# Kernel tuning notes

Hardware: AMD Instinct MI355X
Metric: run time of the kernel (lower is better)

The kernel has to match this reference:

```python
import jax, jax.numpy as jnp
import numpy as np


def _avgpool2(x):
    # 2x2 average pool, stride 2, NHWC
    B, H, W, C = x.shape
    return x.reshape(B, H // 2, 2, W // 2, 2, C).mean(axis=(2, 4))


def setup_inputs() -> dict:
    key = jax.random.key(0)
    ks = jax.random.split(key, 5)
    B, H, W, C = 8, 64, 64, 512
    s = 0.02
    return {
        "x": jax.random.normal(ks[0], (B, H, W, C), dtype=jnp.float32),
        "wf": jax.random.normal(ks[1], (C, C // 8), dtype=jnp.float32) * s,
        "wg": jax.random.normal(ks[2], (C, C // 8), dtype=jnp.float32) * s,
        "wh": jax.random.normal(ks[3], (C, C // 2), dtype=jnp.float32) * s,
        "wo": jax.random.normal(ks[4], (C // 2, C), dtype=jnp.float32) * s,
    }


def reference(x, wf, wg, wh, wo):
    B, H, W, C = x.shape
    # queries from full resolution: 1x1 conv == channel matmul
    f = jnp.einsum("bhwc,cd->bhwd", x, wf).reshape(B, H * W, C // 8)
    # keys/values from 2x2 average-pooled map
    xp = _avgpool2(x)  # [B, H/2, W/2, C]
    g = jnp.einsum("bhwc,cd->bhwd", xp, wg).reshape(B, H * W // 4, C // 8)
    h = jnp.einsum("bhwc,cd->bhwd", xp, wh).reshape(B, H * W // 4, C // 2)
    # attn: [B, HW, HW/4], softmax over pooled key axis
    attn = jax.nn.softmax(jnp.einsum("bnd,bmd->bnm", f, g), axis=-1)
    y = jnp.einsum("bnm,bmd->bnd", attn, h).reshape(B, H, W, C // 2)
    # output 1x1 conv back to C channels
    return jnp.einsum("bhwc,cd->bhwd", y, wo)
```

## Files before the change

### kernel.cpp

```cpp
#include <hip/hip_runtime.h>
#include <hip/hip_bf16.h>

typedef __attribute__((ext_vector_type(8))) short bshort8;
typedef __attribute__((ext_vector_type(4))) float f32x4;
typedef __attribute__((ext_vector_type(4))) float vfloat4;
typedef __attribute__((ext_vector_type(4))) unsigned int vuint4;
typedef __attribute__((ext_vector_type(2))) unsigned int vuint2;

__device__ __forceinline__ unsigned short f2bf(float f) {
    union { float f; unsigned u; } v; v.f = f;
    unsigned u = v.u;
    u += 0x7fffu + ((u >> 16) & 1u);
    return (unsigned short)(u >> 16);
}

template<int EPI>
__global__ __launch_bounds__(256)
void gemm_bt(const unsigned short* __restrict__ Av, const unsigned short* __restrict__ Btv,
             void* __restrict__ Cv,
             int M, int N, int K,
             long long aB, long long bB, long long cB)
{
    __shared__ __align__(128) char sA[64 * 64];
    __shared__ __align__(128) char sB[64 * 64];

    const int b    = blockIdx.z;
    const int tid  = threadIdx.x;
    const int bRow = blockIdx.y << 6;
    const int bCol = blockIdx.x << 6;
    const int wid  = tid >> 6, lane = tid & 63;
    const int wr   = wid >> 1, wc   = wid & 1;
    const int r16  = lane & 15, kg  = lane >> 4;
    const int srow = tid >> 2,  skc = tid & 3;

    const unsigned short* A  = Av  + (size_t)aB * b;
    const unsigned short* Bt = Btv + (size_t)bB * b;

    f32x4 acc[2][2] = {};

    const size_t aRowBase = (size_t)(bRow + srow) * K + skc * 8;
    const size_t bRowBase = (size_t)(bCol + srow) * K + skc * 8;
    const unsigned swW = ((((unsigned)srow) << 6) | (((unsigned)skc) << 4))
                         ^ ((((unsigned)srow) & 7u) << 4);

    for (int k0 = 0; k0 < K; k0 += 32) {
        vuint4 apack = *(const vuint4*)(A  + aRowBase + k0);
        vuint4 bpack = *(const vuint4*)(Bt + bRowBase + k0);
        *(vuint4*)(sA + swW) = apack;
        *(vuint4*)(sB + swW) = bpack;
        __syncthreads();

        bshort8 af[2], bfr[2];
        #pragma unroll
        for (int mi = 0; mi < 2; mi++) {
            unsigned row = (unsigned)(wr * 32 + mi * 16 + r16);
            unsigned off = ((row << 6) | (((unsigned)kg) << 4)) ^ ((row & 7u) << 4);
            af[mi] = *(const bshort8*)(sA + off);
        }
        #pragma unroll
        for (int ni = 0; ni < 2; ni++) {
            unsigned col = (unsigned)(wc * 32 + ni * 16 + r16);
            unsigned off = ((col << 6) | (((unsigned)kg) << 4)) ^ ((col & 7u) << 4);
            bfr[ni] = *(const bshort8*)(sB + off);
        }
        #pragma unroll
        for (int mi = 0; mi < 2; mi++)
            #pragma unroll
            for (int ni = 0; ni < 2; ni++)
                acc[mi][ni] = __builtin_amdgcn_mfma_f32_16x16x32_bf16(
                                  af[mi], bfr[ni], acc[mi][ni], 0, 0, 0);
        __syncthreads();
    }

    #pragma unroll
    for (int mi = 0; mi < 2; mi++) {
        const int row0 = bRow + wr * 32 + mi * 16 + kg * 4;
        #pragma unroll
        for (int ni = 0; ni < 2; ni++) {
            const int col = bCol + wc * 32 + ni * 16 + r16;
            #pragma unroll
            for (int r = 0; r < 4; r++) {
                const int row = row0 + r;
                float x = acc[mi][ni][r];
                const size_t ci = (size_t)cB * b + (size_t)row * N + col;
                if constexpr (EPI == 0) ((float*)Cv)[ci] = x;
                else                    ((unsigned short*)Cv)[ci] = f2bf(x);
            }
        }
    }
}

__global__ __launch_bounds__(512)
void flash_attn(const float* __restrict__ x,
                const unsigned short* __restrict__ wft,
                const unsigned short* __restrict__ gb,
                const unsigned short* __restrict__ ht,
                unsigned short* __restrict__ yb)
{
    __shared__ __align__(128) char sS[128 * 128];
    __shared__ __align__(128) char sG[64 * 128];
    __shared__ __align__(128) char sH[256 * 128];
    __shared__ float rs[128];

    const int tid = threadIdx.x;
    const int bid = blockIdx.x;
    const int b   = bid & 7;
    const int q0  = (bid >> 3) << 7;
    const int wid = tid >> 6, lane = tid & 63;
    const int wr  = wid >> 1, wc = wid & 1;
    const int r16 = lane & 15, kg = lane >> 4;

    const float*          xB = x  + ((size_t)b * 4096 + q0) * 512;
    const unsigned short* gB = gb + (size_t)b * 1024 * 64;
    const unsigned short* hB = ht + (size_t)b * 256 * 1024;

    f32x4 facc[4] = {};
    {
        const int xrow = tid >> 2, xc = tid & 3;
        const int wrow = tid >> 3, wkc = tid & 7;
        const int frow = wid << 4;
        for (int k0 = 0; k0 < 512; k0 += 64) {
            {
                const float* p = xB + (size_t)xrow * 512 + k0 + xc * 16;
                #pragma unroll
                for (int j = 0; j < 2; j++) {
                    vfloat4 a0 = *(const vfloat4*)(p + j * 8);
                    vfloat4 a1 = *(const vfloat4*)(p + j * 8 + 4);
                    vuint4 w;
                    w[0] = (unsigned)f2bf(a0[0]) | ((unsigned)f2bf(a0[1]) << 16);
                    w[1] = (unsigned)f2bf(a0[2]) | ((unsigned)f2bf(a0[3]) << 16);
                    w[2] = (unsigned)f2bf(a1[0]) | ((unsigned)f2bf(a1[1]) << 16);
                    w[3] = (unsigned)f2bf(a1[2]) | ((unsigned)f2bf(a1[3]) << 16);
                    unsigned off = ((unsigned)xrow * 128 + (unsigned)(xc * 32 + j * 16))
                                   ^ (((unsigned)xrow & 7u) << 4);
                    *(vuint4*)(sH + off) = w;
                }
            }
            {
                vuint4 v = *(const vuint4*)(wft + (size_t)wrow * 512 + k0 + wkc * 8);
                unsigned off = ((unsigned)wrow * 128 + (unsigned)wkc * 16)
                               ^ (((unsigned)wrow & 7u) << 4);
                *(vuint4*)(sG + off) = v;
            }
            __syncthreads();

            bshort8 ax[2];
            {
                unsigned row = (unsigned)(frow + r16);
                unsigned base = row * 128, sw = (row & 7u) << 4;
                ax[0] = *(const bshort8*)(sH + ((base + (unsigned)kg * 16) ^ sw));
                ax[1] = *(const bshort8*)(sH + ((base + 64 + (unsigned)kg * 16) ^ sw));
            }
            #pragma unroll
            for (int ni = 0; ni < 4; ni++) {
                unsigned col = (unsigned)(ni * 16 + r16);
                unsigned base = col * 128, sw = (col & 7u) << 4;
                bshort8 b0 = *(const bshort8*)(sG + ((base + (unsigned)kg * 16) ^ sw));
                bshort8 b1 = *(const bshort8*)(sG + ((base + 64 + (unsigned)kg * 16) ^ sw));
                facc[ni] = __builtin_amdgcn_mfma_f32_16x16x32_bf16(ax[0], b0, facc[ni], 0, 0, 0);
                facc[ni] = __builtin_amdgcn_mfma_f32_16x16x32_bf16(ax[1], b1, facc[ni], 0, 0, 0);
            }
            __syncthreads();
        }

        #pragma unroll
        for (int ni = 0; ni < 4; ni++) {
            const unsigned col = (unsigned)(ni * 16 + r16);
            #pragma unroll
            for (int r = 0; r < 4; r++) {
                unsigned row = (unsigned)(frow + kg * 4 + r);
                unsigned off = (row * 128 + col * 2) ^ ((row & 7u) << 4);
                *(unsigned short*)(sS + off) = f2bf(facc[ni][r]);
            }
        }
    }
    __syncthreads();

    bshort8 af[2][2];
    #pragma unroll
    for (int mi = 0; mi < 2; mi++) {
        unsigned row = (unsigned)(wr * 32 + mi * 16 + r16);
        unsigned base = row * 128, sw = (row & 7u) << 4;
        af[mi][0] = *(const bshort8*)(sS + ((base + (unsigned)kg * 16) ^ sw));
        af[mi][1] = *(const bshort8*)(sS + ((base + 64 + (unsigned)kg * 16) ^ sw));
    }

    f32x4 yacc[2][8] = {};
    float psum[2][4] = {};
    const int kc = tid & 7, n0 = tid >> 3;

    for (int c = 0; c < 16; c++) {
        const int kv0 = c << 6;
        {
            vuint4 v = *(const vuint4*)(gB + (size_t)(kv0 + n0) * 64 + kc * 8);
            unsigned off = ((unsigned)n0 * 128 + (unsigned)kc * 16) ^ (((unsigned)n0 & 7u) << 4);
            *(vuint4*)(sG + off) = v;
        }
        #pragma unroll
        for (int it = 0; it < 4; it++) {
            const int n = n0 + it * 64;
            vuint4 v = *(const vuint4*)(hB + (size_t)n * 1024 + kv0 + kc * 8);
            unsigned off = ((unsigned)n * 128 + (unsigned)kc * 16) ^ (((unsigned)n & 7u) << 4);
            *(vuint4*)(sH + off) = v;
        }
        __syncthreads();

        f32x4 sacc[2][2] = {};
        #pragma unroll
        for (int ni = 0; ni < 2; ni++) {
            unsigned col = (unsigned)(wc * 32 + ni * 16 + r16);
            unsigned base = col * 128, sw = (col & 7u) << 4;
            bshort8 g0 = *(const bshort8*)(sG + ((base + (unsigned)kg * 16) ^ sw));
            bshort8 g1 = *(const bshort8*)(sG + ((base + 64 + (unsigned)kg * 16) ^ sw));
            #pragma unroll
            for (int mi = 0; mi < 2; mi++) {
                sacc[mi][ni] = __builtin_amdgcn_mfma_f32_16x16x32_bf16(af[mi][0], g0, sacc[mi][ni], 0, 0, 0);
                sacc[mi][ni] = __builtin_amdgcn_mfma_f32_16x16x32_bf16(af[mi][1], g1, sacc[mi][ni], 0, 0, 0);
            }
        }

        #pragma unroll
        for (int mi = 0; mi < 2; mi++)
            #pragma unroll
            for (int ni = 0; ni < 2; ni++) {
                const unsigned col = (unsigned)(wc * 32 + ni * 16 + r16);
                #pragma unroll
                for (int r = 0; r < 4; r++) {
                    float e = __expf(sacc[mi][ni][r]);
                    psum[mi][r] += e;
                    unsigned row = (unsigned)(wr * 32 + mi * 16 + kg * 4 + r);
                    unsigned off = (row * 128 + col * 2) ^ ((row & 7u) << 4);
                    *(unsigned short*)(sS + off) = f2bf(e);
                }
            }
        __syncthreads();

        bshort8 pa[2][2];
        #pragma unroll
        for (int mi = 0; mi < 2; mi++) {
            unsigned row = (unsigned)(wr * 32 + mi * 16 + r16);
            unsigned base = row * 128, sw = (row & 7u) << 4;
            pa[mi][0] = *(const bshort8*)(sS + ((base + (unsigned)kg * 16) ^ sw));
            pa[mi][1] = *(const bshort8*)(sS + ((base + 64 + (unsigned)kg * 16) ^ sw));
        }
        #pragma unroll
        for (int ni = 0; ni < 8; ni++) {
            unsigned col = (unsigned)(wc * 128 + ni * 16 + r16);
            unsigned base = col * 128, sw = (col & 7u) << 4;
            bshort8 b0 = *(const bshort8*)(sH + ((base + (unsigned)kg * 16) ^ sw));
            bshort8 b1 = *(const bshort8*)(sH + ((base + 64 + (unsigned)kg * 16) ^ sw));
            #pragma unroll
            for (int mi = 0; mi < 2; mi++) {
                yacc[mi][ni] = __builtin_amdgcn_mfma_f32_16x16x32_bf16(pa[mi][0], b0, yacc[mi][ni], 0, 0, 0);
                yacc[mi][ni] = __builtin_amdgcn_mfma_f32_16x16x32_bf16(pa[mi][1], b1, yacc[mi][ni], 0, 0, 0);
            }
        }
        __syncthreads();
    }

    #pragma unroll
    for (int mi = 0; mi < 2; mi++)
        #pragma unroll
        for (int r = 0; r < 4; r++) {
            float s = psum[mi][r];
            s += __shfl_xor(s, 1, 64);
            s += __shfl_xor(s, 2, 64);
            s += __shfl_xor(s, 4, 64);
            s += __shfl_xor(s, 8, 64);
            psum[mi][r] = s;
        }
    if (wc == 0 && r16 == 0) {
        #pragma unroll
        for (int mi = 0; mi < 2; mi++)
            #pragma unroll
            for (int r = 0; r < 4; r++)
                rs[wr * 32 + mi * 16 + kg * 4 + r] = psum[mi][r];
    }
    __syncthreads();
    if (wc == 1 && r16 == 0) {
        #pragma unroll
        for (int mi = 0; mi < 2; mi++)
            #pragma unroll
            for (int r = 0; r < 4; r++)
                rs[wr * 32 + mi * 16 + kg * 4 + r] += psum[mi][r];
    }
    __syncthreads();

    unsigned short* yB = yb + ((size_t)b * 4096 + q0) * 256;
    #pragma unroll
    for (int mi = 0; mi < 2; mi++)
        #pragma unroll
        for (int r = 0; r < 4; r++) {
            const int row = wr * 32 + mi * 16 + kg * 4 + r;
            const float rinv = 1.0f / rs[row];
            #pragma unroll
            for (int ni = 0; ni < 8; ni++) {
                const int col = wc * 128 + ni * 16 + r16;
                yB[(size_t)row * 256 + col] = f2bf(yacc[mi][ni][r] * rinv);
            }
        }
}

__global__ __launch_bounds__(256)
void pool2(const float* __restrict__ x, unsigned short* __restrict__ xp)
{
    const int t  = blockIdx.x * 256 + threadIdx.x;
    const int c4 = t & 127;
    const int j  = (t >> 7) & 31;
    const int i  = (t >> 12) & 31;
    const int b  = t >> 17;
    const float* p = x + ((((size_t)b * 64 + 2 * i) * 64) + 2 * j) * 512 + c4 * 4;
    vfloat4 a0 = *(const vfloat4*)p;
    vfloat4 a1 = *(const vfloat4*)(p + 512);
    vfloat4 a2 = *(const vfloat4*)(p + 64 * 512);
    vfloat4 a3 = *(const vfloat4*)(p + 64 * 512 + 512);
    float r0 = 0.25f * (a0[0] + a1[0] + a2[0] + a3[0]);
    float r1 = 0.25f * (a0[1] + a1[1] + a2[1] + a3[1]);
    float r2 = 0.25f * (a0[2] + a1[2] + a2[2] + a3[2]);
    float r3 = 0.25f * (a0[3] + a1[3] + a2[3] + a3[3]);
    vuint2 o;
    o[0] = (unsigned)f2bf(r0) | ((unsigned)f2bf(r1) << 16);
    o[1] = (unsigned)f2bf(r2) | ((unsigned)f2bf(r3) << 16);
    *(vuint2*)(xp + (size_t)t * 4) = o;
}

__global__ __launch_bounds__(256)
void transpose_cast(const float* __restrict__ in, unsigned short* __restrict__ out,
                    int Kdim, int Ndim)
{
    const int idx = blockIdx.x * 256 + threadIdx.x;
    if (idx >= Kdim * Ndim) return;
    const int n = idx / Kdim, k = idx % Kdim;
    out[idx] = f2bf(in[(size_t)k * Ndim + n]);
}

extern "C" void kernel_launch(void* const* d_in, const int* in_sizes, int n_in,
                              void* d_out, int out_size, void* d_ws, size_t ws_size,
                              hipStream_t stream)
{
    const float* x  = (const float*)d_in[0];
    const float* wf = (const float*)d_in[1];
    const float* wg = (const float*)d_in[2];
    const float* wh = (const float*)d_in[3];
    const float* wo = (const float*)d_in[4];
    float* out = (float*)d_out;

    char* ws = (char*)d_ws;
    size_t off = 0;
    auto carve = [&](size_t bytes) {
        char* p = ws + off;
        off = (off + bytes + 255) & ~(size_t)255;
        return p;
    };
    unsigned short* xp   = (unsigned short*)carve(8ll * 1024 * 512 * 2);
    unsigned short* wf_t = (unsigned short*)carve(64 * 512 * 2);
    unsigned short* wg_t = (unsigned short*)carve(64 * 512 * 2);
    unsigned short* wh_t = (unsigned short*)carve(256 * 512 * 2);
    unsigned short* wo_t = (unsigned short*)carve(512 * 256 * 2);
    unsigned short* gb   = (unsigned short*)carve(8ll * 1024 * 64 * 2);
    unsigned short* ht   = (unsigned short*)carve(8ll * 256 * 1024 * 2);
    unsigned short* yb   = (unsigned short*)carve(8ll * 4096 * 256 * 2);

    transpose_cast<<<dim3(128),  256, 0, stream>>>(wf, wf_t, 512, 64);
    transpose_cast<<<dim3(128),  256, 0, stream>>>(wg, wg_t, 512, 64);
    transpose_cast<<<dim3(512),  256, 0, stream>>>(wh, wh_t, 512, 256);
    transpose_cast<<<dim3(512),  256, 0, stream>>>(wo, wo_t, 256, 512);

    pool2<<<dim3(4096), 256, 0, stream>>>(x, xp);

    gemm_bt<1><<<dim3(1, 128, 1), 256, 0, stream>>>(xp, wg_t, gb, 8192, 64, 512, 0, 0, 0);
    gemm_bt<1><<<dim3(16, 4, 8), 256, 0, stream>>>(wh_t, xp, ht, 256, 1024, 512,
                                                   0, 1024LL * 512, 256LL * 1024);

    flash_attn<<<dim3(256), 512, 0, stream>>>(x, wf_t, gb, ht, yb);

    gemm_bt<0><<<dim3(8, 512, 1), 256, 0, stream>>>(yb, wo_t, out, 32768, 512, 256, 0, 0, 0);
}
```

Baseline: 213.3 us.

## Double-buffer K/V tiles in flash attention and fuse weight transposes

```diff
diff --git a/kernel.cpp b/kernel.cpp
--- a/kernel.cpp
+++ b/kernel.cpp
@@ -98,8 +98,8 @@
                 unsigned short* __restrict__ yb)
 {
     __shared__ __align__(128) char sS[128 * 128];
-    __shared__ __align__(128) char sG[64 * 128];
-    __shared__ __align__(128) char sH[256 * 128];
+    __shared__ __align__(128) char sG[2][64 * 128];
+    __shared__ __align__(128) char sH[2][256 * 128];
     __shared__ float rs[128];
 
     const int tid = threadIdx.x;
@@ -113,6 +113,9 @@
     const float*          xB = x  + ((size_t)b * 4096 + q0) * 512;
     const unsigned short* gB = gb + (size_t)b * 1024 * 64;
     const unsigned short* hB = ht + (size_t)b * 256 * 1024;
+
+    char* const sG0 = sG[0];
+    char* const sH0 = sH[0];
 
     f32x4 facc[4] = {};
     {
@@ -133,14 +136,14 @@
                     w[3] = (unsigned)f2bf(a1[2]) | ((unsigned)f2bf(a1[3]) << 16);
                     unsigned off = ((unsigned)xrow * 128 + (unsigned)(xc * 32 + j * 16))
                                    ^ (((unsigned)xrow & 7u) << 4);
-                    *(vuint4*)(sH + off) = w;
+                    *(vuint4*)(sH0 + off) = w;
                 }
             }
             {
                 vuint4 v = *(const vuint4*)(wft + (size_t)wrow * 512 + k0 + wkc * 8);
                 unsigned off = ((unsigned)wrow * 128 + (unsigned)wkc * 16)
                                ^ (((unsigned)wrow & 7u) << 4);
-                *(vuint4*)(sG + off) = v;
+                *(vuint4*)(sG0 + off) = v;
             }
             __syncthreads();
 
@@ -148,32 +151,49 @@
             {
                 unsigned row = (unsigned)(frow + r16);
                 unsigned base = row * 128, sw = (row & 7u) << 4;
-                ax[0] = *(const bshort8*)(sH + ((base + (unsigned)kg * 16) ^ sw));
-                ax[1] = *(const bshort8*)(sH + ((base + 64 + (unsigned)kg * 16) ^ sw));
+                ax[0] = *(const bshort8*)(sH0 + ((base + (unsigned)kg * 16) ^ sw));
+                ax[1] = *(const bshort8*)(sH0 + ((base + 64 + (unsigned)kg * 16) ^ sw));
             }
             #pragma unroll
             for (int ni = 0; ni < 4; ni++) {
                 unsigned col = (unsigned)(ni * 16 + r16);
                 unsigned base = col * 128, sw = (col & 7u) << 4;
-                bshort8 b0 = *(const bshort8*)(sG + ((base + (unsigned)kg * 16) ^ sw));
-                bshort8 b1 = *(const bshort8*)(sG + ((base + 64 + (unsigned)kg * 16) ^ sw));
+                bshort8 b0 = *(const bshort8*)(sG0 + ((base + (unsigned)kg * 16) ^ sw));
+                bshort8 b1 = *(const bshort8*)(sG0 + ((base + 64 + (unsigned)kg * 16) ^ sw));
                 facc[ni] = __builtin_amdgcn_mfma_f32_16x16x32_bf16(ax[0], b0, facc[ni], 0, 0, 0);
                 facc[ni] = __builtin_amdgcn_mfma_f32_16x16x32_bf16(ax[1], b1, facc[ni], 0, 0, 0);
             }
             __syncthreads();
         }
 
+        const int frow2 = wid << 4;
         #pragma unroll
         for (int ni = 0; ni < 4; ni++) {
             const unsigned col = (unsigned)(ni * 16 + r16);
             #pragma unroll
             for (int r = 0; r < 4; r++) {
-                unsigned row = (unsigned)(frow + kg * 4 + r);
+                unsigned row = (unsigned)(frow2 + kg * 4 + r);
                 unsigned off = (row * 128 + col * 2) ^ ((row & 7u) << 4);
                 *(unsigned short*)(sS + off) = f2bf(facc[ni][r]);
             }
         }
     }
+
+    const int kc = tid & 7, n0 = tid >> 3;
+    const unsigned gOff  = ((unsigned)n0 * 128 + (unsigned)kc * 16) ^ (((unsigned)n0 & 7u) << 4);
+    const unsigned hOff0 = gOff;
+
+    vuint4 gR, hR0, hR1, hR2, hR3;
+    gR  = *(const vuint4*)(gB + (size_t)n0 * 64 + kc * 8);
+    hR0 = *(const vuint4*)(hB + (size_t)(n0      ) * 1024 + kc * 8);
+    hR1 = *(const vuint4*)(hB + (size_t)(n0 +  64) * 1024 + kc * 8);
+    hR2 = *(const vuint4*)(hB + (size_t)(n0 + 128) * 1024 + kc * 8);
+    hR3 = *(const vuint4*)(hB + (size_t)(n0 + 192) * 1024 + kc * 8);
+    *(vuint4*)(sG0 + gOff)               = gR;
+    *(vuint4*)(sH0 + hOff0)              = hR0;
+    *(vuint4*)(sH0 + hOff0 +     8192)   = hR1;
+    *(vuint4*)(sH0 + hOff0 + 2 * 8192)   = hR2;
+    *(vuint4*)(sH0 + hOff0 + 3 * 8192)   = hR3;
     __syncthreads();
 
     bshort8 af[2][2];
@@ -184,34 +204,32 @@
         af[mi][0] = *(const bshort8*)(sS + ((base + (unsigned)kg * 16) ^ sw));
         af[mi][1] = *(const bshort8*)(sS + ((base + 64 + (unsigned)kg * 16) ^ sw));
     }
+    __syncthreads();
 
     f32x4 yacc[2][8] = {};
     float psum[2][4] = {};
-    const int kc = tid & 7, n0 = tid >> 3;
 
     for (int c = 0; c < 16; c++) {
-        const int kv0 = c << 6;
-        {
-            vuint4 v = *(const vuint4*)(gB + (size_t)(kv0 + n0) * 64 + kc * 8);
-            unsigned off = ((unsigned)n0 * 128 + (unsigned)kc * 16) ^ (((unsigned)n0 & 7u) << 4);
-            *(vuint4*)(sG + off) = v;
-        }
-        #pragma unroll
-        for (int it = 0; it < 4; it++) {
-            const int n = n0 + it * 64;
-            vuint4 v = *(const vuint4*)(hB + (size_t)n * 1024 + kv0 + kc * 8);
-            unsigned off = ((unsigned)n * 128 + (unsigned)kc * 16) ^ (((unsigned)n & 7u) << 4);
-            *(vuint4*)(sH + off) = v;
-        }
-        __syncthreads();
+        const int cur = c & 1;
+        char* const sGc = sG[cur];
+        char* const sHc = sH[cur];
+
+        if (c < 15) {
+            const int kv1 = (c + 1) << 6;
+            gR  = *(const vuint4*)(gB + (size_t)(kv1 + n0) * 64 + kc * 8);
+            hR0 = *(const vuint4*)(hB + (size_t)(n0      ) * 1024 + kv1 + kc * 8);
+            hR1 = *(const vuint4*)(hB + (size_t)(n0 +  64) * 1024 + kv1 + kc * 8);
+            hR2 = *(const vuint4*)(hB + (size_t)(n0 + 128) * 1024 + kv1 + kc * 8);
+            hR3 = *(const vuint4*)(hB + (size_t)(n0 + 192) * 1024 + kv1 + kc * 8);
+        }
 
         f32x4 sacc[2][2] = {};
         #pragma unroll
         for (int ni = 0; ni < 2; ni++) {
             unsigned col = (unsigned)(wc * 32 + ni * 16 + r16);
             unsigned base = col * 128, sw = (col & 7u) << 4;
-            bshort8 g0 = *(const bshort8*)(sG + ((base + (unsigned)kg * 16) ^ sw));
-            bshort8 g1 = *(const bshort8*)(sG + ((base + 64 + (unsigned)kg * 16) ^ sw));
+            bshort8 g0 = *(const bshort8*)(sGc + ((base + (unsigned)kg * 16) ^ sw));
+            bshort8 g1 = *(const bshort8*)(sGc + ((base + 64 + (unsigned)kg * 16) ^ sw));
             #pragma unroll
             for (int mi = 0; mi < 2; mi++) {
                 sacc[mi][ni] = __builtin_amdgcn_mfma_f32_16x16x32_bf16(af[mi][0], g0, sacc[mi][ni], 0, 0, 0);
@@ -247,13 +265,23 @@
         for (int ni = 0; ni < 8; ni++) {
             unsigned col = (unsigned)(wc * 128 + ni * 16 + r16);
             unsigned base = col * 128, sw = (col & 7u) << 4;
-            bshort8 b0 = *(const bshort8*)(sH + ((base + (unsigned)kg * 16) ^ sw));
-            bshort8 b1 = *(const bshort8*)(sH + ((base + 64 + (unsigned)kg * 16) ^ sw));
+            bshort8 b0 = *(const bshort8*)(sHc + ((base + (unsigned)kg * 16) ^ sw));
+            bshort8 b1 = *(const bshort8*)(sHc + ((base + 64 + (unsigned)kg * 16) ^ sw));
             #pragma unroll
             for (int mi = 0; mi < 2; mi++) {
                 yacc[mi][ni] = __builtin_amdgcn_mfma_f32_16x16x32_bf16(pa[mi][0], b0, yacc[mi][ni], 0, 0, 0);
                 yacc[mi][ni] = __builtin_amdgcn_mfma_f32_16x16x32_bf16(pa[mi][1], b1, yacc[mi][ni], 0, 0, 0);
             }
+        }
+
+        if (c < 15) {
+            char* const sGn = sG[cur ^ 1];
+            char* const sHn = sH[cur ^ 1];
+            *(vuint4*)(sGn + gOff)             = gR;
+            *(vuint4*)(sHn + hOff0)            = hR0;
+            *(vuint4*)(sHn + hOff0 +     8192) = hR1;
+            *(vuint4*)(sHn + hOff0 + 2 * 8192) = hR2;
+            *(vuint4*)(sHn + hOff0 + 3 * 8192) = hR3;
         }
         __syncthreads();
     }
@@ -325,13 +353,28 @@
 }
 
 __global__ __launch_bounds__(256)
-void transpose_cast(const float* __restrict__ in, unsigned short* __restrict__ out,
-                    int Kdim, int Ndim)
+void wprep(const float* __restrict__ wf, const float* __restrict__ wg,
+           const float* __restrict__ wh, const float* __restrict__ wo,
+           unsigned short* __restrict__ wf_t, unsigned short* __restrict__ wg_t,
+           unsigned short* __restrict__ wh_t, unsigned short* __restrict__ wo_t)
 {
-    const int idx = blockIdx.x * 256 + threadIdx.x;
-    if (idx >= Kdim * Ndim) return;
-    const int n = idx / Kdim, k = idx % Kdim;
-    out[idx] = f2bf(in[(size_t)k * Ndim + n]);
+    __shared__ float tile[32][33];
+    int t = blockIdx.x;
+    const float* in; unsigned short* out; int K, N;
+    if (t < 32)       { in = wf; out = wf_t; K = 512; N = 64;  }
+    else if (t < 64)  { in = wg; out = wg_t; K = 512; N = 64;  t -= 32;  }
+    else if (t < 192) { in = wh; out = wh_t; K = 512; N = 256; t -= 64;  }
+    else              { in = wo; out = wo_t; K = 256; N = 512; t -= 192; }
+    const int ntN = N >> 5;
+    const int tk = (t / ntN) << 5, tn = (t % ntN) << 5;
+    const int tx = threadIdx.x & 31, ty = threadIdx.x >> 5;
+    #pragma unroll
+    for (int s = 0; s < 4; s++)
+        tile[ty + s * 8][tx] = in[(size_t)(tk + ty + s * 8) * N + tn + tx];
+    __syncthreads();
+    #pragma unroll
+    for (int s = 0; s < 4; s++)
+        out[(size_t)(tn + ty + s * 8) * K + tk + tx] = f2bf(tile[tx][ty + s * 8]);
 }
 
 extern "C" void kernel_launch(void* const* d_in, const int* in_sizes, int n_in,
@@ -361,10 +404,7 @@
     unsigned short* ht   = (unsigned short*)carve(8ll * 256 * 1024 * 2);
     unsigned short* yb   = (unsigned short*)carve(8ll * 4096 * 256 * 2);
 
-    transpose_cast<<<dim3(128),  256, 0, stream>>>(wf, wf_t, 512, 64);
-    transpose_cast<<<dim3(128),  256, 0, stream>>>(wg, wg_t, 512, 64);
-    transpose_cast<<<dim3(512),  256, 0, stream>>>(wh, wh_t, 512, 256);
-    transpose_cast<<<dim3(512),  256, 0, stream>>>(wo, wo_t, 256, 512);
+    wprep<<<dim3(320), 256, 0, stream>>>(wf, wg, wh, wo, wf_t, wg_t, wh_t, wo_t);
 
     pool2<<<dim3(4096), 256, 0, stream>>>(x, xp);
 
```

New measurement: 203.3 us. 1.05x faster.
